# Kernel optimization log

Hardware: AMD Instinct MI355X
Metric: run time of the kernel (lower is better)

The kernel has to match this reference:

```python
import jax, jax.numpy as jnp
import numpy as np

B, T = 32, 2048            # batch, longest acoustic length
SIN, HIN = 1024, 1024      # decoder-state dim, listener-output dim
KD, VD = 512, 512          # key/value projection dims
EPS = 1e-12                # F.normalize eps


def setup_inputs() -> dict:
    key = jax.random.key(0)
    ks = jax.random.split(key, 9)
    s = 0.02
    return {
        "decoder_state": jax.random.normal(ks[0], (B, SIN), dtype=jnp.float32),
        "listener_output": jax.random.normal(ks[1], (B, T, HIN), dtype=jnp.float32),
        "outputs_length": jax.random.randint(ks[2], (B,), 1, T + 1, dtype=jnp.int32),
        "Ws": jax.random.normal(ks[3], (KD, SIN), dtype=jnp.float32) * s,
        "bs": jnp.zeros((KD,), dtype=jnp.float32),
        "Wh": jax.random.normal(ks[4], (KD, HIN), dtype=jnp.float32) * s,
        "bh": jnp.zeros((KD,), dtype=jnp.float32),
        "Wv": jax.random.normal(ks[5], (VD, HIN), dtype=jnp.float32) * s,
        "bv": jnp.zeros((VD,), dtype=jnp.float32),
    }


def reference(decoder_state, listener_output, outputs_length, Ws, bs, Wh, bh, Wv, bv):
    # query: [B, KD]
    query = decoder_state @ Ws.T + bs
    # key: [B, T, KD]
    keyp = jnp.einsum('bth,kh->btk', listener_output, Wh) + bh
    # energy: [B, 1, T]
    energy = jnp.einsum('bk,btk->bt', query, keyp)[:, None, :]
    attn = jax.nn.softmax(energy, axis=2)
    # length mask; NOTE: original loop skips i==0, so sample 0 is never masked
    pos = jnp.arange(T)
    mask = (pos[None, :] < outputs_length[:, None]).astype(attn.dtype)
    mask = mask.at[0].set(1.0)
    attn = attn * mask[:, None, :]
    # L1 renormalize (F.normalize p=1, dim=2, eps=1e-12); attn >= 0
    attn = attn / jnp.maximum(jnp.sum(attn, axis=2, keepdims=True), EPS)
    # value: [B, T, VD]; context: [B, VD]
    value = jnp.einsum('bth,vh->btv', listener_output, Wv) + bv
    context = jnp.einsum('bqt,btv->bqv', attn, value)[:, 0, :]
    return context, attn
```

## Files before the change

### kernel.cpp

```cpp
#include <hip/hip_runtime.h>
#include <math.h>

#define BB 32
#define TT 2048
#define SIN 1024
#define HIN 1024
#define KD 512
#define VD 512
#define EBASE 20.0f

#define OFF_Q      0
#define OFF_WPART  16384
#define OFF_E      147456
#define OFF_PART   212992
#define OFF_CTX    1265664
#define OFF_R      1298432

__device__ __forceinline__ float dot4(float4 a, float4 b) {
  return fmaf(a.x, b.x, fmaf(a.y, b.y, fmaf(a.z, b.z, a.w * b.w)));
}

__device__ __forceinline__ float4 add4(float4 a, float4 b) {
  return make_float4(a.x + b.x, a.y + b.y, a.z + b.z, a.w + b.w);
}

__device__ __forceinline__ float wave_reduce_sum(float e) {
#pragma unroll
  for (int off = 32; off > 0; off >>= 1) e += __shfl_xor(e, off, 64);
  return e;
}

__global__ __launch_bounds__(256) void k_query(const float* __restrict__ ds,
                                               const float* __restrict__ Ws,
                                               const float* __restrict__ bs,
                                               float* __restrict__ q) {
  const int lane = threadIdx.x & 63;
  const int wid  = threadIdx.x >> 6;
  const int k    = blockIdx.x * 4 + wid;
  const float4* Wr = (const float4*)(Ws + (size_t)k * SIN);
  float4 w0 = Wr[lane], w1 = Wr[64 + lane], w2 = Wr[128 + lane], w3 = Wr[192 + lane];
  float bk = bs[k];
  for (int b = 0; b < BB; ++b) {
    const float4* dr = (const float4*)(ds + (size_t)b * SIN);
    float4 d0 = dr[lane], d1 = dr[64 + lane], d2 = dr[128 + lane], d3 = dr[192 + lane];
    float e = dot4(w0, d0) + dot4(w1, d1) + dot4(w2, d2) + dot4(w3, d3);
    e = wave_reduce_sum(e);
    if (lane == 0) q[(size_t)b * KD + k] = e + bk;
  }
}

__global__ __launch_bounds__(256) void k_wpart(const float* __restrict__ Wh,
                                               const float* __restrict__ q,
                                               float* __restrict__ wpart) {
  __shared__ float qs[8][128];
  const int h  = blockIdx.x * 256 + threadIdx.x;
  const int b0 = blockIdx.y * 8;
  const int k0 = blockIdx.z * 128;
#pragma unroll
  for (int r = 0; r < 4; ++r) {
    int lin = r * 256 + threadIdx.x;
    qs[lin >> 7][lin & 127] = q[(size_t)(b0 + (lin >> 7)) * KD + k0 + (lin & 127)];
  }
  __syncthreads();
  float acc[8] = {0.f, 0.f, 0.f, 0.f, 0.f, 0.f, 0.f, 0.f};
  for (int kk = 0; kk < 128; ++kk) {
    float wh = Wh[(size_t)(k0 + kk) * HIN + h];
#pragma unroll
    for (int i = 0; i < 8; ++i) acc[i] = fmaf(wh, qs[i][kk], acc[i]);
  }
#pragma unroll
  for (int i = 0; i < 8; ++i)
    wpart[(size_t)blockIdx.z * (BB * HIN) + (size_t)(b0 + i) * HIN + h] = acc[i];
}

__global__ __launch_bounds__(256) void k_main(const float* __restrict__ L,
                                              const float* __restrict__ wpart,
                                              const int* __restrict__ lens,
                                              float* __restrict__ pen,
                                              float* __restrict__ part) {
  const int b     = blockIdx.x >> 5;
  const int chunk = blockIdx.x & 31;
  const int t0    = chunk * 64;
  const int wid   = threadIdx.x >> 6;
  const int lane  = threadIdx.x & 63;
  const int len   = lens[b];
  const bool row0 = (b == 0);

  const float4* q0 = (const float4*)(wpart + (size_t)(0 * BB + b) * HIN);
  const float4* q1 = (const float4*)(wpart + (size_t)(1 * BB + b) * HIN);
  const float4* q2 = (const float4*)(wpart + (size_t)(2 * BB + b) * HIN);
  const float4* q3 = (const float4*)(wpart + (size_t)(3 * BB + b) * HIN);
  float4 w0 = add4(add4(q0[lane],       q1[lane]),       add4(q2[lane],       q3[lane]));
  float4 w1 = add4(add4(q0[64 + lane],  q1[64 + lane]),  add4(q2[64 + lane],  q3[64 + lane]));
  float4 w2 = add4(add4(q0[128 + lane], q1[128 + lane]), add4(q2[128 + lane], q3[128 + lane]));
  float4 w3 = add4(add4(q0[192 + lane], q1[192 + lane]), add4(q2[192 + lane], q3[192 + lane]));

  float z = 0.f, kept = 0.f;
  float4 a0 = {0, 0, 0, 0}, a1 = {0, 0, 0, 0}, a2 = {0, 0, 0, 0}, a3 = {0, 0, 0, 0};
  const size_t rowbase = (size_t)b * TT * HIN;

  __shared__ float hdr[4][2];
  __shared__ float accs[4][1024];
  __shared__ float sp[64];

#pragma unroll 2
  for (int i = 0; i < 16; ++i) {
    const int t = t0 + i * 4 + wid;
    const float4* vr = (const float4*)(L + rowbase + (size_t)t * HIN);
    float4 v0 = vr[lane], v1 = vr[64 + lane], v2 = vr[128 + lane], v3 = vr[192 + lane];
    float e = dot4(w0, v0) + dot4(w1, v1) + dot4(w2, v2) + dot4(w3, v3);
    e = wave_reduce_sum(e);
    float p = __expf(e - EBASE);
    if (lane == 0) sp[i * 4 + wid] = p;
    float g = (row0 || t < len) ? p : 0.f;
    z += p;
    kept += g;
    a0.x = fmaf(g, v0.x, a0.x); a0.y = fmaf(g, v0.y, a0.y);
    a0.z = fmaf(g, v0.z, a0.z); a0.w = fmaf(g, v0.w, a0.w);
    a1.x = fmaf(g, v1.x, a1.x); a1.y = fmaf(g, v1.y, a1.y);
    a1.z = fmaf(g, v1.z, a1.z); a1.w = fmaf(g, v1.w, a1.w);
    a2.x = fmaf(g, v2.x, a2.x); a2.y = fmaf(g, v2.y, a2.y);
    a2.z = fmaf(g, v2.z, a2.z); a2.w = fmaf(g, v2.w, a2.w);
    a3.x = fmaf(g, v3.x, a3.x); a3.y = fmaf(g, v3.y, a3.y);
    a3.w = fmaf(g, v3.w, a3.w); a3.z = fmaf(g, v3.z, a3.z);
  }

  if (lane == 0) { hdr[wid][0] = z; hdr[wid][1] = kept; }
  float4* as = (float4*)accs[wid];
  as[lane] = a0; as[64 + lane] = a1; as[128 + lane] = a2; as[192 + lane] = a3;
  __syncthreads();
  float* pb = part + (size_t)blockIdx.x * 1028;
  if (threadIdx.x == 0) {
    pb[0] = hdr[0][0] + hdr[1][0] + hdr[2][0] + hdr[3][0];
    pb[1] = hdr[0][1] + hdr[1][1] + hdr[2][1] + hdr[3][1];
  }
  if (threadIdx.x < 64) pen[(size_t)b * TT + t0 + threadIdx.x] = sp[threadIdx.x];
#pragma unroll
  for (int i = 0; i < 4; ++i) {
    int h = threadIdx.x + 256 * i;
    pb[4 + h] = accs[0][h] + accs[1][h] + accs[2][h] + accs[3][h];
  }
}

__global__ __launch_bounds__(256) void k_reduce(const float* __restrict__ part,
                                                const float* __restrict__ pen,
                                                const int* __restrict__ lens,
                                                float* __restrict__ ctx,
                                                float* __restrict__ rb,
                                                float* __restrict__ out_attn) {
  const int b = blockIdx.x >> 2;
  const int s = blockIdx.x & 3;
  __shared__ float sZ[32], sK[32];
  if (threadIdx.x < 32) {
    const float* pb = part + (size_t)(b * 32 + threadIdx.x) * 1028;
    sZ[threadIdx.x] = pb[0]; sK[threadIdx.x] = pb[1];
  }
  __syncthreads();
  float Z = 0.f, K = 0.f;
#pragma unroll
  for (int i = 0; i < 32; ++i) { Z += sZ[i]; K += sK[i]; }
  const float kept_sum = K / Z;
  const float ks = fmaxf(kept_sum, 1e-12f);
  const float inv = 1.f / (Z * ks);
  const int h = s * 256 + threadIdx.x;
  float A = 0.f;
#pragma unroll
  for (int p = 0; p < 32; ++p)
    A += part[(size_t)(b * 32 + p) * 1028 + 4 + h];
  ctx[(size_t)b * HIN + h] = A * inv;
  const int len = lens[b];
#pragma unroll
  for (int j = 0; j < 2; ++j) {
    int t = s * 512 + j * 256 + threadIdx.x;
    bool keep = (b == 0) || (t < len);
    float pe = pen[(size_t)b * TT + t];
    out_attn[(size_t)b * TT + t] = keep ? pe * inv : 0.f;
  }
  if (s == 0 && threadIdx.x == 0) rb[b] = kept_sum / ks;
}

__global__ __launch_bounds__(256) void k_context(const float* __restrict__ Wvm,
                                                 const float* __restrict__ bv,
                                                 const float* __restrict__ ctx,
                                                 const float* __restrict__ rb,
                                                 float* __restrict__ out) {
  const int lane = threadIdx.x & 63;
  const int wid  = threadIdx.x >> 6;
  const int v    = blockIdx.x * 4 + wid;
  const float4* Wr = (const float4*)(Wvm + (size_t)v * HIN);
  float4 w0 = Wr[lane], w1 = Wr[64 + lane], w2 = Wr[128 + lane], w3 = Wr[192 + lane];
  const float bvv = bv[v];
  for (int b = 0; b < BB; ++b) {
    const float4* cr = (const float4*)(ctx + (size_t)b * HIN);
    float4 c0 = cr[lane], c1 = cr[64 + lane], c2 = cr[128 + lane], c3 = cr[192 + lane];
    float e = dot4(w0, c0) + dot4(w1, c1) + dot4(w2, c2) + dot4(w3, c3);
    e = wave_reduce_sum(e);
    if (lane == 0) out[(size_t)b * VD + v] = e + bvv * rb[b];
  }
}

extern "C" void kernel_launch(void* const* d_in, const int* in_sizes, int n_in,
                              void* d_out, int out_size, void* d_ws, size_t ws_size,
                              hipStream_t stream) {
  const float* ds   = (const float*)d_in[0];
  const float* L    = (const float*)d_in[1];
  const int*   lens = (const int*)d_in[2];
  const float* Ws   = (const float*)d_in[3];
  const float* bs   = (const float*)d_in[4];
  const float* Wh   = (const float*)d_in[5];
  const float* Wv   = (const float*)d_in[7];
  const float* bv   = (const float*)d_in[8];
  float* out = (float*)d_out;
  float* ws  = (float*)d_ws;

  float* q      = ws + OFF_Q;
  float* wpart  = ws + OFF_WPART;
  float* pen    = ws + OFF_E;
  float* part   = ws + OFF_PART;
  float* ctx    = ws + OFF_CTX;
  float* rbuf   = ws + OFF_R;

  k_query  <<<128, 256, 0, stream>>>(ds, Ws, bs, q);
  k_wpart  <<<dim3(4, 4, 4), 256, 0, stream>>>(Wh, q, wpart);
  k_main   <<<1024, 256, 0, stream>>>(L, wpart, lens, pen, part);
  k_reduce <<<128, 256, 0, stream>>>(part, pen, lens, ctx, rbuf, out + BB * VD);
  k_context<<<128, 256, 0, stream>>>(Wv, bv, ctx, rbuf, out);
}
```

Baseline: 438.3 us.

## Fuse context projection into reduce kernel and drop split-K partials for query weights

The Wh-times-query kernel now covers the full K dimension in each block, so it writes one weight vector per batch instead of four partials that the main kernel had to sum. The reduce and context-projection kernels are merged: each block keeps the normalized context row in shared memory and applies its slice of Wv directly. This removes one launch and the ctx/rb round trip through global memory. In exchange, k_w runs with only 16 blocks over a serial 512-long loop, and each k_fin block reads 128 rows of Wv, so Wv is re-read once per batch element.

```diff
diff --git a/kernel.cpp b/kernel.cpp
--- a/kernel.cpp
+++ b/kernel.cpp
@@ -10,11 +10,9 @@
 #define EBASE 20.0f
 
 #define OFF_Q      0
-#define OFF_WPART  16384
-#define OFF_E      147456
-#define OFF_PART   212992
-#define OFF_CTX    1265664
-#define OFF_R      1298432
+#define OFF_W      16384
+#define OFF_E      49152
+#define OFF_PART   114688
 
 __device__ __forceinline__ float dot4(float4 a, float4 b) {
   return fmaf(a.x, b.x, fmaf(a.y, b.y, fmaf(a.z, b.z, a.w * b.w)));
@@ -49,32 +47,31 @@
   }
 }
 
-__global__ __launch_bounds__(256) void k_wpart(const float* __restrict__ Wh,
-                                               const float* __restrict__ q,
-                                               float* __restrict__ wpart) {
-  __shared__ float qs[8][128];
+__global__ __launch_bounds__(256) void k_w(const float* __restrict__ Wh,
+                                           const float* __restrict__ q,
+                                           float* __restrict__ w) {
+  __shared__ float qs[8][KD];
   const int h  = blockIdx.x * 256 + threadIdx.x;
   const int b0 = blockIdx.y * 8;
-  const int k0 = blockIdx.z * 128;
-#pragma unroll
-  for (int r = 0; r < 4; ++r) {
+#pragma unroll
+  for (int r = 0; r < 16; ++r) {
     int lin = r * 256 + threadIdx.x;
-    qs[lin >> 7][lin & 127] = q[(size_t)(b0 + (lin >> 7)) * KD + k0 + (lin & 127)];
+    qs[lin >> 9][lin & 511] = q[(size_t)(b0 + (lin >> 9)) * KD + (lin & 511)];
   }
   __syncthreads();
   float acc[8] = {0.f, 0.f, 0.f, 0.f, 0.f, 0.f, 0.f, 0.f};
-  for (int kk = 0; kk < 128; ++kk) {
-    float wh = Wh[(size_t)(k0 + kk) * HIN + h];
+  for (int kk = 0; kk < KD; ++kk) {
+    float wh = Wh[(size_t)kk * HIN + h];
 #pragma unroll
     for (int i = 0; i < 8; ++i) acc[i] = fmaf(wh, qs[i][kk], acc[i]);
   }
 #pragma unroll
   for (int i = 0; i < 8; ++i)
-    wpart[(size_t)blockIdx.z * (BB * HIN) + (size_t)(b0 + i) * HIN + h] = acc[i];
+    w[(size_t)(b0 + i) * HIN + h] = acc[i];
 }
 
 __global__ __launch_bounds__(256) void k_main(const float* __restrict__ L,
-                                              const float* __restrict__ wpart,
+                                              const float* __restrict__ wv,
                                               const int* __restrict__ lens,
                                               float* __restrict__ pen,
                                               float* __restrict__ part) {
@@ -86,14 +83,8 @@
   const int len   = lens[b];
   const bool row0 = (b == 0);
 
-  const float4* q0 = (const float4*)(wpart + (size_t)(0 * BB + b) * HIN);
-  const float4* q1 = (const float4*)(wpart + (size_t)(1 * BB + b) * HIN);
-  const float4* q2 = (const float4*)(wpart + (size_t)(2 * BB + b) * HIN);
-  const float4* q3 = (const float4*)(wpart + (size_t)(3 * BB + b) * HIN);
-  float4 w0 = add4(add4(q0[lane],       q1[lane]),       add4(q2[lane],       q3[lane]));
-  float4 w1 = add4(add4(q0[64 + lane],  q1[64 + lane]),  add4(q2[64 + lane],  q3[64 + lane]));
-  float4 w2 = add4(add4(q0[128 + lane], q1[128 + lane]), add4(q2[128 + lane], q3[128 + lane]));
-  float4 w3 = add4(add4(q0[192 + lane], q1[192 + lane]), add4(q2[192 + lane], q3[192 + lane]));
+  const float4* wr = (const float4*)(wv + (size_t)b * HIN);
+  float4 w0 = wr[lane], w1 = wr[64 + lane], w2 = wr[128 + lane], w3 = wr[192 + lane];
 
   float z = 0.f, kept = 0.f;
   float4 a0 = {0, 0, 0, 0}, a1 = {0, 0, 0, 0}, a2 = {0, 0, 0, 0}, a3 = {0, 0, 0, 0};
@@ -122,7 +113,7 @@
     a2.x = fmaf(g, v2.x, a2.x); a2.y = fmaf(g, v2.y, a2.y);
     a2.z = fmaf(g, v2.z, a2.z); a2.w = fmaf(g, v2.w, a2.w);
     a3.x = fmaf(g, v3.x, a3.x); a3.y = fmaf(g, v3.y, a3.y);
-    a3.w = fmaf(g, v3.w, a3.w); a3.z = fmaf(g, v3.z, a3.z);
+    a3.z = fmaf(g, v3.z, a3.z); a3.w = fmaf(g, v3.w, a3.w);
   }
 
   if (lane == 0) { hdr[wid][0] = z; hdr[wid][1] = kept; }
@@ -142,15 +133,19 @@
   }
 }
 
-__global__ __launch_bounds__(256) void k_reduce(const float* __restrict__ part,
-                                                const float* __restrict__ pen,
-                                                const int* __restrict__ lens,
-                                                float* __restrict__ ctx,
-                                                float* __restrict__ rb,
-                                                float* __restrict__ out_attn) {
+__global__ __launch_bounds__(256) void k_fin(const float* __restrict__ part,
+                                             const float* __restrict__ pen,
+                                             const int* __restrict__ lens,
+                                             const float* __restrict__ Wvm,
+                                             const float* __restrict__ bv,
+                                             float* __restrict__ out,
+                                             float* __restrict__ out_attn) {
   const int b = blockIdx.x >> 2;
   const int s = blockIdx.x & 3;
+  const int lane = threadIdx.x & 63;
+  const int wid  = threadIdx.x >> 6;
   __shared__ float sZ[32], sK[32];
+  __shared__ float sc[1024];
   if (threadIdx.x < 32) {
     const float* pb = part + (size_t)(b * 32 + threadIdx.x) * 1028;
     sZ[threadIdx.x] = pb[0]; sK[threadIdx.x] = pb[1];
@@ -162,12 +157,14 @@
   const float kept_sum = K / Z;
   const float ks = fmaxf(kept_sum, 1e-12f);
   const float inv = 1.f / (Z * ks);
-  const int h = s * 256 + threadIdx.x;
-  float A = 0.f;
+  const float rbv = kept_sum / ks;
+
+  float4 A = {0.f, 0.f, 0.f, 0.f};
 #pragma unroll
   for (int p = 0; p < 32; ++p)
-    A += part[(size_t)(b * 32 + p) * 1028 + 4 + h];
-  ctx[(size_t)b * HIN + h] = A * inv;
+    A = add4(A, *(const float4*)(part + (size_t)(b * 32 + p) * 1028 + 4 + threadIdx.x * 4));
+  ((float4*)sc)[threadIdx.x] = make_float4(A.x * inv, A.y * inv, A.z * inv, A.w * inv);
+
   const int len = lens[b];
 #pragma unroll
   for (int j = 0; j < 2; ++j) {
@@ -176,26 +173,17 @@
     float pe = pen[(size_t)b * TT + t];
     out_attn[(size_t)b * TT + t] = keep ? pe * inv : 0.f;
   }
-  if (s == 0 && threadIdx.x == 0) rb[b] = kept_sum / ks;
-}
-
-__global__ __launch_bounds__(256) void k_context(const float* __restrict__ Wvm,
-                                                 const float* __restrict__ bv,
-                                                 const float* __restrict__ ctx,
-                                                 const float* __restrict__ rb,
-                                                 float* __restrict__ out) {
-  const int lane = threadIdx.x & 63;
-  const int wid  = threadIdx.x >> 6;
-  const int v    = blockIdx.x * 4 + wid;
-  const float4* Wr = (const float4*)(Wvm + (size_t)v * HIN);
-  float4 w0 = Wr[lane], w1 = Wr[64 + lane], w2 = Wr[128 + lane], w3 = Wr[192 + lane];
-  const float bvv = bv[v];
-  for (int b = 0; b < BB; ++b) {
-    const float4* cr = (const float4*)(ctx + (size_t)b * HIN);
-    float4 c0 = cr[lane], c1 = cr[64 + lane], c2 = cr[128 + lane], c3 = cr[192 + lane];
+  __syncthreads();
+
+  const float4* scv = (const float4*)sc;
+  float4 c0 = scv[lane], c1 = scv[64 + lane], c2 = scv[128 + lane], c3 = scv[192 + lane];
+  for (int j = 0; j < 32; ++j) {
+    const int v = s * 128 + wid * 32 + j;
+    const float4* Wr = (const float4*)(Wvm + (size_t)v * HIN);
+    float4 w0 = Wr[lane], w1 = Wr[64 + lane], w2 = Wr[128 + lane], w3 = Wr[192 + lane];
     float e = dot4(w0, c0) + dot4(w1, c1) + dot4(w2, c2) + dot4(w3, c3);
     e = wave_reduce_sum(e);
-    if (lane == 0) out[(size_t)b * VD + v] = e + bvv * rb[b];
+    if (lane == 0) out[(size_t)b * VD + v] = e + bv[v] * rbv;
   }
 }
 
@@ -213,16 +201,13 @@
   float* out = (float*)d_out;
   float* ws  = (float*)d_ws;
 
-  float* q      = ws + OFF_Q;
-  float* wpart  = ws + OFF_WPART;
-  float* pen    = ws + OFF_E;
-  float* part   = ws + OFF_PART;
-  float* ctx    = ws + OFF_CTX;
-  float* rbuf   = ws + OFF_R;
-
-  k_query  <<<128, 256, 0, stream>>>(ds, Ws, bs, q);
-  k_wpart  <<<dim3(4, 4, 4), 256, 0, stream>>>(Wh, q, wpart);
-  k_main   <<<1024, 256, 0, stream>>>(L, wpart, lens, pen, part);
-  k_reduce <<<128, 256, 0, stream>>>(part, pen, lens, ctx, rbuf, out + BB * VD);
-  k_context<<<128, 256, 0, stream>>>(Wv, bv, ctx, rbuf, out);
-}
+  float* q    = ws + OFF_Q;
+  float* w    = ws + OFF_W;
+  float* pen  = ws + OFF_E;
+  float* part = ws + OFF_PART;
+
+  k_query<<<128, 256, 0, stream>>>(ds, Ws, bs, q);
+  k_w    <<<dim3(4, 4), 256, 0, stream>>>(Wh, q, w);
+  k_main <<<1024, 256, 0, stream>>>(L, w, lens, pen, part);
+  k_fin  <<<128, 256, 0, stream>>>(part, pen, lens, Wv, bv, out, out + BB * VD);
+}
```

Measured after the change: 466.7 us. +6.5%, slower.
